# Performance work log

Hardware: AMD Instinct MI355X
Metric: run time of the kernel (lower is better)

## Reference

```python
import jax, jax.numpy as jnp
import numpy as np

# LSR-Patch tokenizer config (matches init_kwargs / torch defaults)
SPEC_WINDOW = 32
SPEC_HOP = 8
PELT_PENALTY = 1.0
PATCH_MIN = 8
PATCH_MAX = 64
PATCH_GRID = 2
ANCHOR_LEN = 16
ALPHA = 1.0
BETA = 1.0

B, C, L = 32, 64, 8192

# ---------------- host-side (numpy) planning: boundaries, segment stats, patch layout ----------------
# These produce integer index structures (non-differentiable in the torch original too:
# regime/center/span are built from python floats via torch.tensor -> constant leaves).

def _window_feats(agg):
    Ln = agg.shape[0]
    W = min(SPEC_WINDOW, Ln)
    if Ln <= W:
        starts = [0]
    else:
        starts = list(range(0, Ln - W + 1, SPEC_HOP))
        if starts[-1] != Ln - W:
            starts.append(Ln - W)
    s = np.asarray(starts)
    frames = agg[s[:, None] + np.arange(W)[None, :]]           # [n_win, W]
    p = np.abs(np.fft.rfft(frames, axis=1)) ** 2
    p = p[:, 1:]                                                # drop DC
    tot = np.maximum(p.sum(1), 1e-8)
    dom = np.argmax(p, 1) + 1
    f = np.arange(1, p.shape[1] + 1, dtype=np.float64)
    cent = (p * f).sum(1) / tot
    var = ((f[None, :] - cent[:, None]) ** 2 * p).sum(1) / tot
    bw = np.sqrt(np.maximum(var, 0.0)) / float(W)
    feat = np.stack([dom / float(W), bw, np.log1p(p.mean(1))], 1)
    return feat, starts

def _dp_changepoints(feat):
    # penalized DP (simplified PELT), O(n^2), vectorized inner minimization
    n, d = feat.shape
    pre = np.vstack([np.zeros((1, d)), np.cumsum(feat, 0)])
    pre2 = np.vstack([np.zeros((1, d)), np.cumsum(feat ** 2, 0)])
    dp = np.full(n + 1, np.inf)
    dp[0] = -PELT_PENALTY
    prev = np.full(n + 1, -1, np.int64)
    for end in range(1, n + 1):
        sl = (end - np.arange(end)).astype(np.float64)
        ssum = pre[end] - pre[:end]
        ssq = pre2[end] - pre2[:end]
        sse = (ssq - ssum ** 2 / sl[:, None]).sum(1)
        cand = dp[:end] + sse + PELT_PENALTY
        j = int(np.argmin(cand))
        dp[end] = cand[j]
        prev[end] = j
    bps = [n]
    i = n
    while i > 0:
        i = int(prev[i])
        bps.append(i)
    return bps[::-1]

def _detect_boundaries(agg):
    Ln = agg.shape[0]
    if Ln <= max(2, PATCH_MIN):
        return [0, Ln]
    feat, ws = _window_feats(agg)
    if feat.shape[0] <= 1:
        return [0, Ln]
    wb = _dp_changepoints(feat)
    bnd = [0]
    for w in wb[1:-1]:
        if w < 0 or w >= len(ws):
            continue
        t = int(ws[w])
        if t <= bnd[-1] or t - bnd[-1] < PATCH_MIN or Ln - t < PATCH_MIN:
            continue
        bnd.append(t)
    bnd.append(Ln)
    return bnd

def _segment_stats(seg):
    n = seg.shape[0]
    if n < 2:
        return 1.0, 0.0
    p = np.abs(np.fft.rfft(seg)) ** 2
    if p.size <= 1:
        return float(n), 0.0
    p = p[1:]
    tot = max(p.sum(), 1e-8)
    dom = int(np.argmax(p)) + 1
    f = np.arange(1, p.size + 1, dtype=np.float64)
    cent = (p * f).sum() / tot
    var = ((f - cent) ** 2 * p).sum() / tot
    bw = float(np.sqrt(max(var, 0.0)) / n)
    return float(n) / dom, bw

def _gen_patch_len(dom_period, bw, seg_len):
    # reconstruction of _generate_patch_length (truncated in source):
    # patch length ~ alpha*dom_period shrunk by bandwidth, snapped to grid, clamped
    raw = ALPHA * dom_period / (1.0 + BETA * bw)
    p = int(round(raw / PATCH_GRID)) * PATCH_GRID
    p = min(max(p, PATCH_MIN), PATCH_MAX)
    return max(1, p)

def _resize_plan(start, end):
    # F.interpolate(mode='linear', align_corners=False) gather indices + weights
    n = end - start
    A = ANCHOR_LEN
    src = (np.arange(A) + 0.5) * (n / float(A)) - 0.5
    src = np.clip(src, 0.0, n - 1.0)
    i0 = np.floor(src).astype(np.int64)
    i1 = np.minimum(i0 + 1, n - 1)
    w = (src - i0).astype(np.float32)
    return start + i0, start + i1, w

def _plan(x_np):
    Bn, Cn, Ln = x_np.shape
    plans = []
    mx = 0
    for b in range(Bn):
        agg = x_np[b].mean(0).astype(np.float64)
        bnd = _detect_boundaries(agg)
        i0s, i1s, ws, st, en, ce, sp, rg = [], [], [], [], [], [], [], []
        for s, e in zip(bnd[:-1], bnd[1:]):
            if e <= s:
                continue
            dom_p, bw = _segment_stats(agg[s:e])
            pl = _gen_patch_len(dom_p, bw, e - s)
            reg = [dom_p / float(max(Ln, 1)), bw, (e - s) / float(max(Ln, 1))]
            for a in range(s, e, pl):
                z = min(e, a + pl)
                if z <= a:
                    continue
                g0, g1, wv = _resize_plan(a, z)
                i0s.append(g0); i1s.append(g1); ws.append(wv)
                st.append(a); en.append(z)
                ce.append((a + z - 1) * 0.5 / float(Ln - 1) if Ln > 1 else 0.0)
                sp.append((z - a) / float(max(Ln, 1)))
                rg.append(reg)
        plans.append(dict(i0=np.stack(i0s), i1=np.stack(i1s), w=np.stack(ws),
                          start=np.asarray(st, np.int32), end=np.asarray(en, np.int32),
                          center=np.asarray(ce, np.float32), span=np.asarray(sp, np.float32),
                          regime=np.asarray(rg, np.float32), n=len(st)))
        mx = max(mx, len(st))
    return plans, mx

# ---------------- device-side (jnp) patch extraction: one batched gather+lerp per sample ----------------

def _patches(x, plans, mx):
    outs = []
    for b, p in enumerate(plans):
        w = jnp.asarray(p['w'])                                   # [n, A]
        g = x[b][:, p['i0']] * (1.0 - w) + x[b][:, p['i1']] * w    # [C, n, A]
        g = jnp.transpose(g, (1, 0, 2))                            # [n, C, A]
        outs.append(jnp.pad(g, ((0, mx - p['n']), (0, 0), (0, 0))))
    return jnp.stack(outs, 0)                                      # [B, mx, C, A]

def setup_inputs() -> dict:
    key = jax.random.key(0)
    x = jax.random.normal(key, (B, C, L), dtype=jnp.float32)
    return {"x": x}

def reference(x):
    xn = np.asarray(jax.device_get(x), dtype=np.float32)
    plans, mx = _plan(xn)
    patches = _patches(x, plans, mx)
    token_mask = jnp.stack([jnp.arange(mx) < p['n'] for p in plans], 0)
    start = jnp.stack([jnp.pad(jnp.asarray(p['start']), (0, mx - p['n'])) for p in plans], 0)
    end = jnp.stack([jnp.pad(jnp.asarray(p['end']), (0, mx - p['n'])) for p in plans], 0)
    center = jnp.stack([jnp.pad(jnp.asarray(p['center']), (0, mx - p['n'])) for p in plans], 0)[..., None]
    span = jnp.stack([jnp.pad(jnp.asarray(p['span']), (0, mx - p['n'])) for p in plans], 0)[..., None]
    regime = jnp.stack([jnp.pad(jnp.asarray(p['regime']), ((0, mx - p['n']), (0, 0))) for p in plans], 0)
    n_tokens = jnp.asarray([p['n'] for p in plans], dtype=jnp.int32)
    return (patches, token_mask, start, end, center, span, regime, n_tokens)
```

## Files before the change

### kernel.cpp

```cpp
#include <hip/hip_runtime.h>
#include <math.h>

#pragma clang fp contract(off)

#define BB 32
#define CC 64
#define LL 8192
#define NW 1021
#define MAXSEG 1024
#define MAXTOK 1024
#define BNDCAP 1026
#define NBINS (LL / 2)

#define DP_T 64
#define DP_NBLK 16
#define DP_NWAVE 16
#define DP_MARGIN 1e-6

template <typename F>
__device__ double np_pairwise(const F& f, int off, int n) {
  if (n < 8) {
    double res = 0.0;
    for (int i = 0; i < n; i++) res = res + f(off + i);
    return res;
  }
  if (n <= 128) {
    double r0 = f(off + 0), r1 = f(off + 1), r2 = f(off + 2), r3 = f(off + 3);
    double r4 = f(off + 4), r5 = f(off + 5), r6 = f(off + 6), r7 = f(off + 7);
    int i = 8;
    int lim = n - (n % 8);
    for (; i < lim; i += 8) {
      r0 = r0 + f(off + i + 0); r1 = r1 + f(off + i + 1);
      r2 = r2 + f(off + i + 2); r3 = r3 + f(off + i + 3);
      r4 = r4 + f(off + i + 4); r5 = r5 + f(off + i + 5);
      r6 = r6 + f(off + i + 6); r7 = r7 + f(off + i + 7);
    }
    double res = ((r0 + r1) + (r2 + r3)) + ((r4 + r5) + (r6 + r7));
    for (; i < n; i++) res = res + f(off + i);
    return res;
  }
  int n2 = n / 2;
  n2 -= n2 % 8;
  return np_pairwise(f, off, n2) + np_pairwise(f, off + n2, n - n2);
}

template <int KIND>
__device__ __noinline__ double wp_leaf(const double* __restrict__ pp, double cent,
                                       int off, int n, int lane) {
  int k = lane & 7;
  auto f = [&](int i) -> double {
    double pv = pp[i];
    if constexpr (KIND == 0) {
      return pv;
    } else if constexpr (KIND == 1) {
      return pv * (double)(i + 1);
    } else {
      double d = (double)(i + 1) - cent;
      double dd = d * d;
      return dd * pv;
    }
  };
  double r = f(off + k);
  int lim = n - (n % 8);
  for (int i = 8; i < lim; i += 8) r = r + f(off + i + k);
  double a = r + __shfl_xor(r, 1, 64);
  double b2 = a + __shfl_xor(a, 2, 64);
  double res = b2 + __shfl_xor(b2, 4, 64);
  for (int i = lim; i < n; i++) res = res + f(off + i);
  return res;
}

template <int DEPTH, int KIND>
__device__ double wp_tree(const double* __restrict__ pp, double cent, int off,
                          int n, int lane) {
  if (n <= 128) return wp_leaf<KIND>(pp, cent, off, n, lane);
  if constexpr (DEPTH > 0) {
    int n2 = n / 2;
    n2 -= n2 % 8;
    double l = wp_tree<DEPTH - 1, KIND>(pp, cent, off, n2, lane);
    double r = wp_tree<DEPTH - 1, KIND>(pp, cent, off + n2, n - n2, lane);
    return l + r;
  } else {
    if constexpr (KIND == 0)
      return np_pairwise([&](int i) { return pp[i]; }, off, n);
    else if constexpr (KIND == 1)
      return np_pairwise([&](int i) { return pp[i] * (double)(i + 1); }, off, n);
    else
      return np_pairwise(
          [&](int i) {
            double d = (double)(i + 1) - cent;
            double dd = d * d;
            return dd * pp[i];
          },
          off, n);
  }
}

__global__ void k_agg(const float* __restrict__ x, double* __restrict__ agg) {
  int idx = blockIdx.x * blockDim.x + threadIdx.x;
  if (idx >= BB * LL) return;
  int b = idx / LL, l = idx - b * LL;
  const float* xb = x + (size_t)b * CC * LL + l;
  float s = 0.0f;
  for (int c = 0; c < CC; c++) s = s + xb[(size_t)c * LL];
  agg[idx] = (double)(s / 64.0f);
}

__global__ void k_winfeat(const double* __restrict__ agg, double* __restrict__ feat) {
  __shared__ double tc[32], tsn[32];
  if (threadIdx.x < 32) {
    double th = 6.283185307179586 * ((double)threadIdx.x / 32.0);
    tc[threadIdx.x] = cos(th);
    tsn[threadIdx.x] = sin(th);
  }
  __syncthreads();
  int idx = blockIdx.x * blockDim.x + threadIdx.x;
  if (idx >= BB * NW) return;
  int b = idx / NW, w = idx - b * NW;
  const double* a = agg + (size_t)b * LL + (size_t)w * 8;
  double av[32];
#pragma unroll
  for (int t = 0; t < 32; t++) av[t] = a[t];
  double p[16];
  for (int k = 1; k <= 16; k++) {
    double re = 0.0, im = 0.0;
    int m = 0;
    for (int t = 0; t < 32; t++) {
      re = re + av[t] * tc[m];
      im = im + av[t] * tsn[m];
      m = (m + k) & 31;
    }
    p[k - 1] = re * re + im * im;
  }
  double r[8];
  for (int i = 0; i < 8; i++) r[i] = p[i] + p[i + 8];
  double sum = ((r[0] + r[1]) + (r[2] + r[3])) + ((r[4] + r[5]) + (r[6] + r[7]));
  double tot = (sum > 1e-8) ? sum : 1e-8;
  double pf[16];
  for (int i = 0; i < 16; i++) pf[i] = p[i] * (double)(i + 1);
  for (int i = 0; i < 8; i++) r[i] = pf[i] + pf[i + 8];
  double spf = ((r[0] + r[1]) + (r[2] + r[3])) + ((r[4] + r[5]) + (r[6] + r[7]));
  int dom = 0;
  double bv = p[0];
  for (int i = 1; i < 16; i++)
    if (p[i] > bv) { bv = p[i]; dom = i; }
  dom += 1;
  double cent = spf / tot;
  double q[16];
  for (int i = 0; i < 16; i++) {
    double d = (double)(i + 1) - cent;
    double dd = d * d;
    q[i] = dd * p[i];
  }
  for (int i = 0; i < 8; i++) r[i] = q[i] + q[i + 8];
  double sv = ((r[0] + r[1]) + (r[2] + r[3])) + ((r[4] + r[5]) + (r[6] + r[7]));
  double var = sv / tot;
  double bw = sqrt(var > 0.0 ? var : 0.0) / 32.0;
  double mean = sum / 16.0;
  double* f = feat + ((size_t)b * NW + (size_t)w) * 3;
  f[0] = (double)dom / 32.0;
  f[1] = bw;
  f[2] = log1p(mean);
}

__global__ __launch_bounds__(1024) void k_dp(const double* __restrict__ feat,
                                             int* __restrict__ bnd_g,
                                             int* __restrict__ nbnd_g,
                                             int* __restrict__ seg_s,
                                             int* __restrict__ seg_e,
                                             int* __restrict__ nseg_g) {
  __shared__ double cmb[NW + 1][8];
  __shared__ double sseT[2][DP_T][DP_T + 1];
  __shared__ double pvL[DP_T][DP_NWAVE + 1];
  __shared__ int pixL[DP_T][DP_NWAVE + 1];
  __shared__ int prevL[NW + 1];
  __shared__ double invL[NW + 1];
  int b = blockIdx.x;
  int tid = threadIdx.x;
  const double* fb = feat + (size_t)b * NW * 3;

  double* featS = &sseT[0][0][0];
  for (int i = tid; i < NW * 3; i += 1024) featS[i] = fb[i];
  for (int i = tid + 1; i <= NW; i += 1024) invL[i] = 1.0 / (double)i;
  if (tid == 0) {
    cmb[0][0] = 0.0; cmb[0][1] = 0.0; cmb[0][2] = 0.0;
    cmb[0][3] = 0.0;
    cmb[0][4] = -1.0;
    cmb[0][5] = 0.0; cmb[0][6] = 0.0; cmb[0][7] = 0.0;
  }
  __syncthreads();

  if (tid < 6) {
    int c = tid % 3;
    bool sq = tid >= 3;
    int col = sq ? 5 + c : c;
    double acc = 0.0;
    for (int i = 0; i < NW; i++) {
      double f = featS[i * 3 + c];
      double v = sq ? f * f : f;
      acc = acc + v;
      cmb[i + 1][col] = acc;
    }
  }
  __syncthreads();

  int lane = tid & 63;
  int w = tid >> 6;

  for (int i = tid + 1; i <= NW; i += 1024)
    cmb[i][3] = (cmb[i][5] + cmb[i][6]) + cmb[i][7];
  {
    int end = 1 + lane;
    double pe0 = cmb[end][0], pe1 = cmb[end][1], pe2 = cmb[end][2];
    double qe0 = cmb[end][5], qe1 = cmb[end][6], qe2 = cmb[end][7];
    for (int s = w; s < DP_T; s += DP_NWAVE) {
      int j = s;
      double sl = (double)(end - j);
      double s0 = pe0 - cmb[j][0], s1 = pe1 - cmb[j][1], s2 = pe2 - cmb[j][2];
      double u0 = s0 * s0, u1 = s1 * s1, u2 = s2 * s2;
      double t0 = (qe0 - cmb[j][5]) - u0 / sl;
      double t1 = (qe1 - cmb[j][6]) - u1 / sl;
      double t2 = (qe2 - cmb[j][7]) - u2 / sl;
      sseT[0][s][lane] = (t0 + t1) + t2;
    }
  }
  __syncthreads();

  double dpLast = -1.0;

  for (int blk = 0; blk < DP_NBLK; blk++) {
    int cur = blk & 1, nxt = cur ^ 1;
    int e0 = blk * DP_T;
    int ecnt = NW - e0;
    if (ecnt > DP_T) ecnt = DP_T;
    int end = e0 + 1 + lane;
    if (end > NW) end = NW;
    double pe0 = cmb[end][0], pe1 = cmb[end][1], pe2 = cmb[end][2];
    double qeS = cmb[end][3];
    double vminA = __builtin_inf();
    for (int j = w; j < e0; j += DP_NWAVE) {
      double p0 = cmb[j][0], p1 = cmb[j][1], p2 = cmb[j][2];
      double qs = cmb[j][3], dpj = cmb[j][4];
      double inv = invL[end - j];
      double s0 = pe0 - p0, s1 = pe1 - p1, s2 = pe2 - p2;
      double u0 = s0 * s0, u1 = s1 * s1, u2 = s2 * s2;
      double us = (u0 + u1) + u2;
      double ds = qeS - qs;
      double candA = (dpj + (ds - us * inv)) + 1.0;
      if (candA < vminA) vminA = candA;
    }
    pvL[lane][w] = vminA;
    __syncthreads();
    double mA = pvL[lane][0];
#pragma unroll
    for (int t = 1; t < DP_NWAVE; t++) {
      double ov = pvL[lane][t];
      if (ov < mA) mA = ov;
    }
    double thr = mA + DP_MARGIN;
    __syncthreads();
    double v = __builtin_inf();
    int ix = 0;
    for (int j = w; j < e0; j += DP_NWAVE) {
      double p0 = cmb[j][0], p1 = cmb[j][1], p2 = cmb[j][2];
      double qs = cmb[j][3], dpj = cmb[j][4];
      double inv = invL[end - j];
      double s0 = pe0 - p0, s1 = pe1 - p1, s2 = pe2 - p2;
      double u0 = s0 * s0, u1 = s1 * s1, u2 = s2 * s2;
      double us = (u0 + u1) + u2;
      double ds = qeS - qs;
      double candA = (dpj + (ds - us * inv)) + 1.0;
      if (candA <= thr) {
        double qe0 = cmb[end][5], qe1 = cmb[end][6], qe2 = cmb[end][7];
        double q0 = cmb[j][5], q1 = cmb[j][6], q2 = cmb[j][7];
        double sl = (double)(end - j);
        double t0 = (qe0 - q0) - u0 / sl;
        double t1 = (qe1 - q1) - u1 / sl;
        double t2 = (qe2 - q2) - u2 / sl;
        double cand = (dpj + ((t0 + t1) + t2)) + 1.0;
        if (cand < v || (cand == v && j < ix)) { v = cand; ix = j; }
      }
    }
    pvL[lane][w] = v;
    pixL[lane][w] = ix;
    __syncthreads();
    if (w == 0) {
      double vcur = pvL[lane][0];
      int ixcur = pixL[lane][0];
#pragma unroll
      for (int t = 1; t < DP_NWAVE; t++) {
        double ov = pvL[lane][t];
        int oi = pixL[lane][t];
        if (ov < vcur || (ov == vcur && oi < ixcur)) { vcur = ov; ixcur = oi; }
      }
      double sse_next = sseT[cur][0][lane];
      for (int s = 0; s < ecnt; s++) {
        double sse_cur = sse_next;
        if (s + 1 < ecnt) sse_next = sseT[cur][s + 1][lane];
        double dpj = (s == 0) ? dpLast : __shfl(vcur, s - 1, 64);
        double cand = (dpj + sse_cur) + 1.0;
        if (lane >= s && cand < vcur) { vcur = cand; ixcur = e0 + s; }
        if (lane == s) {
          cmb[end][4] = vcur;
          prevL[end] = ixcur;
        }
      }
      dpLast = __shfl(vcur, ecnt - 1, 64);
    } else if (blk + 1 < DP_NBLK) {
      int e0n = e0 + DP_T;
      int ecn = NW - e0n;
      if (ecn > DP_T) ecn = DP_T;
      int endn = e0n + 1 + lane;
      if (endn > NW) endn = NW;
      double pn0 = cmb[endn][0], pn1 = cmb[endn][1], pn2 = cmb[endn][2];
      double qn0 = cmb[endn][5], qn1 = cmb[endn][6], qn2 = cmb[endn][7];
      for (int s = w - 1; s < ecn; s += DP_NWAVE - 1) {
        int j = e0n + s;
        double sl = (double)(endn - j);
        double s0 = pn0 - cmb[j][0], s1 = pn1 - cmb[j][1], s2 = pn2 - cmb[j][2];
        double u0 = s0 * s0, u1 = s1 * s1, u2 = s2 * s2;
        double t0 = (qn0 - cmb[j][5]) - u0 / sl;
        double t1 = (qn1 - cmb[j][6]) - u1 / sl;
        double t2 = (qn2 - cmb[j][7]) - u2 / sl;
        sseT[nxt][s][lane] = (t0 + t1) + t2;
      }
    }
    __syncthreads();
  }

  if (tid == 0) {
    int* chain = (int*)cmb;
    int cnt = 0, i = NW;
    while (i > 0) { i = prevL[i]; chain[cnt++] = i; }
    int* bbL = (int*)invL;
    int nb = 0;
    bbL[nb++] = 0;
    for (int t = cnt - 2; t >= 0; t--) {
      int w2 = chain[t];
      int tt = w2 * 8;
      if (tt <= bbL[nb - 1]) continue;
      if (tt - bbL[nb - 1] < 8) continue;
      if (LL - tt < 8) continue;
      bbL[nb++] = tt;
    }
    bbL[nb++] = LL;
    int* bb = bnd_g + (size_t)b * BNDCAP;
    for (int t = 0; t < nb; t++) bb[t] = bbL[t];
    nbnd_g[b] = nb;
    int nseg = nb - 1;
    nseg_g[b] = nseg;
    for (int si = 0; si < nseg; si++) {
      seg_s[(size_t)b * MAXSEG + si] = bbL[si];
      seg_e[(size_t)b * MAXSEG + si] = bbL[si + 1];
    }
  }
}

__global__ __launch_bounds__(512) void k_bins(const double* __restrict__ agg,
                                              const int* __restrict__ bnd_g,
                                              const int* __restrict__ nbnd_g,
                                              double* __restrict__ segp) {
#pragma clang fp contract(fast)
  __shared__ int bbS[BNDCAP];
  __shared__ double reS[512], imS[512];
  int b = blockIdx.y;
  int nb = nbnd_g[b];
  for (int i = threadIdx.x; i < nb; i += 512) bbS[i] = bnd_g[(size_t)b * BNDCAP + i];
  __syncthreads();
  int gl = threadIdx.x & 255;
  int h = threadIdx.x >> 8;
  int g = blockIdx.x * 256 + gl;
  int pos = g * 2;
  int lo = 0, hi = nb - 1;
  while (hi - lo > 1) {
    int mid = (lo + hi) >> 1;
    if (bbS[mid] <= pos) lo = mid; else hi = mid;
  }
  int s = bbS[lo], e = bbS[lo + 1];
  int n = e - s;
  int k = g - s / 2 + 1;
  int m = n >> 1;
  const double* ab = agg + (size_t)b * LL + s + h * m;
  double th = 6.283185307179586 * ((double)k / (double)n);
  double cth = cos(th), sth = sin(th);
  double c2 = 2.0 * cth;
  double s1 = 0.0, s2 = 0.0;
  for (int t = m - 4; t >= 0; t -= 4) {
    double a0 = ab[t + 0], a1 = ab[t + 1], a2 = ab[t + 2], a3 = ab[t + 3];
    double x0 = (a3 - s2) + c2 * s1;
    double x1 = (a2 - s1) + c2 * x0;
    double x2 = (a1 - x0) + c2 * x1;
    double x3 = (a0 - x1) + c2 * x2;
    s2 = x2; s1 = x3;
  }
  double re = s1 - cth * s2;
  double im = sth * s2;
  reS[threadIdx.x] = re;
  imS[threadIdx.x] = im;
  __syncthreads();
  if (h == 0) {
    double re1 = reS[256 + gl], im1 = imS[256 + gl];
    double sgn = (k & 1) ? -1.0 : 1.0;
    double rr = re + sgn * re1;
    double ii = im + sgn * im1;
    segp[(size_t)b * NBINS + g] = rr * rr + ii * ii;
  }
}

__global__ __launch_bounds__(256) void k_segfin(
    const double* __restrict__ segp, const int* __restrict__ seg_s,
    const int* __restrict__ seg_e, const int* __restrict__ nseg_g,
    int* __restrict__ seg_pl, double* __restrict__ seg_domp,
    double* __restrict__ seg_bw) {
  __shared__ double ppS[NBINS];
  int b = blockIdx.x;
  for (int i = threadIdx.x; i < NBINS; i += 256) ppS[i] = segp[(size_t)b * NBINS + i];
  __syncthreads();
  int ns = nseg_g[b];
  int lane = threadIdx.x & 63;
  int wid = threadIdx.x >> 6;
  for (int si = wid; si < ns; si += 4) {
    int s = seg_s[(size_t)b * MAXSEG + si];
    int e = seg_e[(size_t)b * MAXSEG + si];
    int n = e - s;
    int nb2 = n / 2;
    int base = s / 2;
    double domp, bwv;
    if (n < 2) {
      domp = 1.0; bwv = 0.0;
    } else if (nb2 <= 1) {
      domp = (double)n; bwv = 0.0;
    } else {
      const double* pp = ppS + base;
      double sum, spf, sv;
      if (nb2 < 8) {
        sum = 0.0;
        for (int i = 0; i < nb2; i++) sum = sum + pp[i];
      } else {
        sum = wp_tree<7, 0>(pp, 0.0, 0, nb2, lane);
      }
      double tot = (sum > 1e-8) ? sum : 1e-8;
      int ch = (nb2 + 63) >> 6;
      double bv = -1.0;
      int bi = 0x7fffffff;
      int st = lane * ch;
      int en2 = st + ch;
      if (en2 > nb2) en2 = nb2;
      if (st < nb2) {
        bv = pp[st]; bi = st;
        for (int i = st + 1; i < en2; i++) {
          double pv = pp[i];
          if (pv > bv) { bv = pv; bi = i; }
        }
      }
      for (int o = 32; o; o >>= 1) {
        double ov = __shfl_xor(bv, o, 64);
        int oi = __shfl_xor(bi, o, 64);
        if (ov > bv || (ov == bv && oi < bi)) { bv = ov; bi = oi; }
      }
      int dom = bi + 1;
      if (nb2 < 8) {
        spf = 0.0;
        for (int i = 0; i < nb2; i++) spf = spf + pp[i] * (double)(i + 1);
      } else {
        spf = wp_tree<7, 1>(pp, 0.0, 0, nb2, lane);
      }
      double cent = spf / tot;
      if (nb2 < 8) {
        sv = 0.0;
        for (int i = 0; i < nb2; i++) {
          double d = (double)(i + 1) - cent;
          double dd = d * d;
          sv = sv + dd * pp[i];
        }
      } else {
        sv = wp_tree<7, 2>(pp, cent, 0, nb2, lane);
      }
      double var = sv / tot;
      bwv = sqrt(var > 0.0 ? var : 0.0) / (double)n;
      domp = (double)n / (double)dom;
    }
    double raw = (1.0 * domp) / (1.0 + 1.0 * bwv);
    int pl = (int)rint(raw / 2.0) * 2;
    if (pl < 8) pl = 8;
    if (pl > 64) pl = 64;
    if (lane == 0) {
      seg_pl[(size_t)b * MAXSEG + si] = pl;
      seg_domp[(size_t)b * MAXSEG + si] = domp;
      seg_bw[(size_t)b * MAXSEG + si] = bwv;
    }
  }
}

__global__ void k_tokens(const int* __restrict__ seg_s, const int* __restrict__ seg_e,
                         const int* __restrict__ seg_pl, const int* __restrict__ nseg_g,
                         int* __restrict__ tok_a, int* __restrict__ tok_z,
                         int* __restrict__ tok_sg, int* __restrict__ ntok_g,
                         float* __restrict__ out_nt) {
  int b = blockIdx.x * blockDim.x + threadIdx.x;
  if (b >= BB) return;
  int ns = nseg_g[b];
  int cnt = 0;
  for (int si = 0; si < ns; si++) {
    int s = seg_s[(size_t)b * MAXSEG + si];
    int e = seg_e[(size_t)b * MAXSEG + si];
    int pl = seg_pl[(size_t)b * MAXSEG + si];
    for (int a = s; a < e; a += pl) {
      int z = a + pl;
      if (z > e) z = e;
      tok_a[(size_t)b * MAXTOK + cnt] = a;
      tok_z[(size_t)b * MAXTOK + cnt] = z;
      tok_sg[(size_t)b * MAXTOK + cnt] = si;
      cnt++;
    }
  }
  ntok_g[b] = cnt;
  out_nt[b] = (float)cnt;
}

__global__ void k_tokfill(const int* __restrict__ tok_a, const int* __restrict__ tok_z,
                          const int* __restrict__ tok_sg, const int* __restrict__ ntok_g,
                          const int* __restrict__ seg_s, const int* __restrict__ seg_e,
                          const double* __restrict__ seg_domp,
                          const double* __restrict__ seg_bw, float* __restrict__ out,
                          int mx) {
  int b = blockIdx.x;
  int t = blockIdx.y * blockDim.x + threadIdx.x;
  if (t >= mx) return;
  size_t BM = (size_t)BB * (size_t)mx;
  float* mask = out + BM * 1024;
  float* start = mask + BM;
  float* endo = start + BM;
  float* cen = endo + BM;
  float* span = cen + BM;
  float* reg = span + BM;
  size_t o = (size_t)b * (size_t)mx + t;
  if (t >= ntok_g[b]) {
    mask[o] = 0.0f; start[o] = 0.0f; endo[o] = 0.0f;
    cen[o] = 0.0f; span[o] = 0.0f;
    reg[o * 3 + 0] = 0.0f; reg[o * 3 + 1] = 0.0f; reg[o * 3 + 2] = 0.0f;
    return;
  }
  int a = tok_a[(size_t)b * MAXTOK + t];
  int z = tok_z[(size_t)b * MAXTOK + t];
  int si = tok_sg[(size_t)b * MAXTOK + t];
  mask[o] = 1.0f;
  start[o] = (float)a;
  endo[o] = (float)z;
  cen[o] = (float)(((double)(a + z - 1) * 0.5) / 8191.0);
  span[o] = (float)((double)(z - a) / 8192.0);
  int s = seg_s[(size_t)b * MAXSEG + si];
  int e = seg_e[(size_t)b * MAXSEG + si];
  reg[o * 3 + 0] = (float)(seg_domp[(size_t)b * MAXSEG + si] / 8192.0);
  reg[o * 3 + 1] = (float)seg_bw[(size_t)b * MAXSEG + si];
  reg[o * 3 + 2] = (float)((double)(e - s) / 8192.0);
}

__global__ __launch_bounds__(256) void k_patches(const float* __restrict__ x,
                                                 const int* __restrict__ tok_a,
                                                 const int* __restrict__ tok_z,
                                                 const int* __restrict__ ntok_g,
                                                 float* __restrict__ out, int mx) {
  int t = blockIdx.x, b = blockIdx.y;
  float* ob = out + (((size_t)b * (size_t)mx + t) * CC) * 16;
  if (t >= ntok_g[b]) {
    for (int e2 = threadIdx.x; e2 < CC * 16; e2 += 256) ob[e2] = 0.0f;
    return;
  }
  __shared__ int g0[16], g1[16];
  __shared__ float wS[16];
  if (threadIdx.x < 16) {
    int a = tok_a[(size_t)b * MAXTOK + t];
    int z = tok_z[(size_t)b * MAXTOK + t];
    int n = z - a;
    double src = ((double)threadIdx.x + 0.5) * ((double)n / 16.0) - 0.5;
    if (src < 0.0) src = 0.0;
    double hi = (double)n - 1.0;
    if (src > hi) src = hi;
    double fi = floor(src);
    int i0 = (int)fi;
    int i1 = i0 + 1;
    if (i1 > n - 1) i1 = n - 1;
    g0[threadIdx.x] = a + i0;
    g1[threadIdx.x] = a + i1;
    wS[threadIdx.x] = (float)(src - fi);
  }
  __syncthreads();
  const float* xb = x + (size_t)b * CC * LL;
  for (int e2 = threadIdx.x; e2 < CC * 16; e2 += 256) {
    int c = e2 >> 4, ai = e2 & 15;
    float wv = wS[ai];
    float v0 = xb[(size_t)c * LL + g0[ai]];
    float v1 = xb[(size_t)c * LL + g1[ai]];
    ob[e2] = v0 * (1.0f - wv) + v1 * wv;
  }
}

extern "C" void kernel_launch(void* const* d_in, const int* in_sizes, int n_in,
                              void* d_out, int out_size, void* d_ws, size_t ws_size,
                              hipStream_t stream) {
  (void)in_sizes; (void)n_in; (void)ws_size;
  const float* x = (const float*)d_in[0];
  float* out = (float*)d_out;
  long mx = ((long)out_size / BB - 1) / 1032;
  if (mx < 1) mx = 1;

  char* wp = (char*)d_ws;
  size_t off = 0;
  auto carve = [&](size_t bytes) -> void* {
    void* p = wp + off;
    off += (bytes + 255) & ~(size_t)255;
    return p;
  };
  double* agg = (double*)carve((size_t)BB * LL * 8);
  double* feat = (double*)carve((size_t)BB * NW * 3 * 8);
  double* segp = (double*)carve((size_t)BB * NBINS * 8);
  double* seg_domp = (double*)carve((size_t)BB * MAXSEG * 8);
  double* seg_bw = (double*)carve((size_t)BB * MAXSEG * 8);
  int* bnd = (int*)carve((size_t)BB * BNDCAP * 4);
  int* nbnd = (int*)carve((size_t)BB * 4);
  int* seg_s = (int*)carve((size_t)BB * MAXSEG * 4);
  int* seg_e = (int*)carve((size_t)BB * MAXSEG * 4);
  int* seg_pl = (int*)carve((size_t)BB * MAXSEG * 4);
  int* nseg = (int*)carve((size_t)BB * 4);
  int* tok_a = (int*)carve((size_t)BB * MAXTOK * 4);
  int* tok_z = (int*)carve((size_t)BB * MAXTOK * 4);
  int* tok_sg = (int*)carve((size_t)BB * MAXTOK * 4);
  int* ntok = (int*)carve((size_t)BB * 4);

  k_agg<<<(BB * LL + 255) / 256, 256, 0, stream>>>(x, agg);
  k_winfeat<<<(BB * NW + 255) / 256, 256, 0, stream>>>(agg, feat);
  k_dp<<<BB, 1024, 0, stream>>>(feat, bnd, nbnd, seg_s, seg_e, nseg);
  dim3 gb(NBINS / 256, BB);
  k_bins<<<gb, 512, 0, stream>>>(agg, bnd, nbnd, segp);
  k_segfin<<<BB, 256, 0, stream>>>(segp, seg_s, seg_e, nseg, seg_pl, seg_domp,
                                   seg_bw);
  k_tokens<<<1, 64, 0, stream>>>(seg_s, seg_e, seg_pl, nseg, tok_a, tok_z,
                                 tok_sg, ntok, out + (size_t)BB * (size_t)mx * 1032);
  dim3 gf(BB, (unsigned)((mx + 255) / 256));
  k_tokfill<<<gf, 256, 0, stream>>>(tok_a, tok_z, tok_sg, ntok, seg_s, seg_e,
                                    seg_domp, seg_bw, out, (int)mx);
  dim3 gp((unsigned)mx, BB);
  k_patches<<<gp, 256, 0, stream>>>(x, tok_a, tok_z, ntok, out, (int)mx);
}
```

Measured before the change: 1.003 ms.

## Pipeline DP candidate scan for next block behind serial wave-0 recurrence

Restructures the blocked changepoint DP so the waves other than wave 0 compute the next block's candidate minima over already-finalized predecessors while wave 0 runs the serial in-block recurrence. The two barrier-separated scan passes per block go away. The current block's contributions are handled by 8 waves after the barrier. Precomputed per-j terms (dp+1-q sum) are folded into cmb[3], and a top-two screening step skips the exact re-evaluation when the best candidate is separated by more than the margin. This reduces barriers and redundant approximate-cost passes, but it adds FMA-based screening whose rounding could change tie-breaking relative to the reference.

```diff
diff --git a/kernel.cpp b/kernel.cpp
--- a/kernel.cpp
+++ b/kernel.cpp
@@ -14,7 +14,6 @@
 
 #define DP_T 64
 #define DP_NBLK 16
-#define DP_NWAVE 16
 #define DP_MARGIN 1e-6
 
 template <typename F>
@@ -170,9 +169,9 @@
                                              int* __restrict__ seg_e,
                                              int* __restrict__ nseg_g) {
   __shared__ double cmb[NW + 1][8];
-  __shared__ double sseT[2][DP_T][DP_T + 1];
-  __shared__ double pvL[DP_T][DP_NWAVE + 1];
-  __shared__ int pixL[DP_T][DP_NWAVE + 1];
+  __shared__ double sseT[2][DP_T][DP_T];
+  __shared__ double pvL[24][DP_T];
+  __shared__ int pixL[24][DP_T];
   __shared__ int prevL[NW + 1];
   __shared__ double invL[NW + 1];
   int b = blockIdx.x;
@@ -182,6 +181,10 @@
   double* featS = &sseT[0][0][0];
   for (int i = tid; i < NW * 3; i += 1024) featS[i] = fb[i];
   for (int i = tid + 1; i <= NW; i += 1024) invL[i] = 1.0 / (double)i;
+  for (int i = tid; i < 24 * DP_T; i += 1024) {
+    (&pvL[0][0])[i] = __builtin_inf();
+    (&pixL[0][0])[i] = 0;
+  }
   if (tid == 0) {
     cmb[0][0] = 0.0; cmb[0][1] = 0.0; cmb[0][2] = 0.0;
     cmb[0][3] = 0.0;
@@ -207,20 +210,17 @@
   int lane = tid & 63;
   int w = tid >> 6;
 
-  for (int i = tid + 1; i <= NW; i += 1024)
-    cmb[i][3] = (cmb[i][5] + cmb[i][6]) + cmb[i][7];
   {
     int end = 1 + lane;
     double pe0 = cmb[end][0], pe1 = cmb[end][1], pe2 = cmb[end][2];
     double qe0 = cmb[end][5], qe1 = cmb[end][6], qe2 = cmb[end][7];
-    for (int s = w; s < DP_T; s += DP_NWAVE) {
-      int j = s;
-      double sl = (double)(end - j);
-      double s0 = pe0 - cmb[j][0], s1 = pe1 - cmb[j][1], s2 = pe2 - cmb[j][2];
+    for (int s = w; s < DP_T; s += 16) {
+      double sl = (double)(end - s);
+      double s0 = pe0 - cmb[s][0], s1 = pe1 - cmb[s][1], s2 = pe2 - cmb[s][2];
       double u0 = s0 * s0, u1 = s1 * s1, u2 = s2 * s2;
-      double t0 = (qe0 - cmb[j][5]) - u0 / sl;
-      double t1 = (qe1 - cmb[j][6]) - u1 / sl;
-      double t2 = (qe2 - cmb[j][7]) - u2 / sl;
+      double t0 = (qe0 - cmb[s][5]) - u0 / sl;
+      double t1 = (qe1 - cmb[s][6]) - u1 / sl;
+      double t2 = (qe2 - cmb[s][7]) - u2 / sl;
       sseT[0][s][lane] = (t0 + t1) + t2;
     }
   }
@@ -233,66 +233,22 @@
     int e0 = blk * DP_T;
     int ecnt = NW - e0;
     if (ecnt > DP_T) ecnt = DP_T;
-    int end = e0 + 1 + lane;
-    if (end > NW) end = NW;
-    double pe0 = cmb[end][0], pe1 = cmb[end][1], pe2 = cmb[end][2];
-    double qeS = cmb[end][3];
-    double vminA = __builtin_inf();
-    for (int j = w; j < e0; j += DP_NWAVE) {
-      double p0 = cmb[j][0], p1 = cmb[j][1], p2 = cmb[j][2];
-      double qs = cmb[j][3], dpj = cmb[j][4];
-      double inv = invL[end - j];
-      double s0 = pe0 - p0, s1 = pe1 - p1, s2 = pe2 - p2;
-      double u0 = s0 * s0, u1 = s1 * s1, u2 = s2 * s2;
-      double us = (u0 + u1) + u2;
-      double ds = qeS - qs;
-      double candA = (dpj + (ds - us * inv)) + 1.0;
-      if (candA < vminA) vminA = candA;
-    }
-    pvL[lane][w] = vminA;
-    __syncthreads();
-    double mA = pvL[lane][0];
+    bool hasNext = (blk + 1 < DP_NBLK);
+    double vBig = __builtin_inf();
+    int ixBig = 0;
+
+    if (w == 0) {
+      int end = e0 + 1 + lane;
+      if (end > NW) end = NW;
+      double vcur = pvL[0][lane];
+      int ixcur = pixL[0][lane];
 #pragma unroll
-    for (int t = 1; t < DP_NWAVE; t++) {
-      double ov = pvL[lane][t];
-      if (ov < mA) mA = ov;
-    }
-    double thr = mA + DP_MARGIN;
-    __syncthreads();
-    double v = __builtin_inf();
-    int ix = 0;
-    for (int j = w; j < e0; j += DP_NWAVE) {
-      double p0 = cmb[j][0], p1 = cmb[j][1], p2 = cmb[j][2];
-      double qs = cmb[j][3], dpj = cmb[j][4];
-      double inv = invL[end - j];
-      double s0 = pe0 - p0, s1 = pe1 - p1, s2 = pe2 - p2;
-      double u0 = s0 * s0, u1 = s1 * s1, u2 = s2 * s2;
-      double us = (u0 + u1) + u2;
-      double ds = qeS - qs;
-      double candA = (dpj + (ds - us * inv)) + 1.0;
-      if (candA <= thr) {
-        double qe0 = cmb[end][5], qe1 = cmb[end][6], qe2 = cmb[end][7];
-        double q0 = cmb[j][5], q1 = cmb[j][6], q2 = cmb[j][7];
-        double sl = (double)(end - j);
-        double t0 = (qe0 - q0) - u0 / sl;
-        double t1 = (qe1 - q1) - u1 / sl;
-        double t2 = (qe2 - q2) - u2 / sl;
-        double cand = (dpj + ((t0 + t1) + t2)) + 1.0;
-        if (cand < v || (cand == v && j < ix)) { v = cand; ix = j; }
-      }
-    }
-    pvL[lane][w] = v;
-    pixL[lane][w] = ix;
-    __syncthreads();
-    if (w == 0) {
-      double vcur = pvL[lane][0];
-      int ixcur = pixL[lane][0];
-#pragma unroll
-      for (int t = 1; t < DP_NWAVE; t++) {
-        double ov = pvL[lane][t];
-        int oi = pixL[lane][t];
+      for (int t = 1; t < 23; t++) {
+        double ov = pvL[t][lane];
+        int oi = pixL[t][lane];
         if (ov < vcur || (ov == vcur && oi < ixcur)) { vcur = ov; ixcur = oi; }
       }
+      double qsE = (cmb[end][5] + cmb[end][6]) + cmb[end][7];
       double sse_next = sseT[cur][0][lane];
       for (int s = 0; s < ecnt; s++) {
         double sse_cur = sse_next;
@@ -303,10 +259,11 @@
         if (lane == s) {
           cmb[end][4] = vcur;
           prevL[end] = ixcur;
+          cmb[end][3] = (vcur + 1.0) - qsE;
         }
       }
       dpLast = __shfl(vcur, ecnt - 1, 64);
-    } else if (blk + 1 < DP_NBLK) {
+    } else if (hasNext) {
       int e0n = e0 + DP_T;
       int ecn = NW - e0n;
       if (ecn > DP_T) ecn = DP_T;
@@ -314,7 +271,7 @@
       if (endn > NW) endn = NW;
       double pn0 = cmb[endn][0], pn1 = cmb[endn][1], pn2 = cmb[endn][2];
       double qn0 = cmb[endn][5], qn1 = cmb[endn][6], qn2 = cmb[endn][7];
-      for (int s = w - 1; s < ecn; s += DP_NWAVE - 1) {
+      for (int s = w - 1; s < ecn; s += 15) {
         int j = e0n + s;
         double sl = (double)(endn - j);
         double s0 = pn0 - cmb[j][0], s1 = pn1 - cmb[j][1], s2 = pn2 - cmb[j][2];
@@ -323,6 +280,121 @@
         double t1 = (qn1 - cmb[j][6]) - u1 / sl;
         double t2 = (qn2 - cmb[j][7]) - u2 / sl;
         sseT[nxt][s][lane] = (t0 + t1) + t2;
+      }
+      double qeS = (qn0 + qn1) + qn2;
+      double m1 = __builtin_inf(), m2 = __builtin_inf();
+      int ix1 = -1;
+      for (int j = w - 1; j < e0; j += 15) {
+        double p0 = cmb[j][0], p1 = cmb[j][1], p2 = cmb[j][2], wj = cmb[j][3];
+        double inv = invL[endn - j];
+        double s0 = pn0 - p0, s1 = pn1 - p1, s2 = pn2 - p2;
+        double us = fma(s2, s2, fma(s1, s1, s0 * s0));
+        double candA = fma(-us, inv, wj + qeS);
+        if (candA < m1) { m2 = m1; m1 = candA; ix1 = j; }
+        else if (candA < m2) { m2 = candA; }
+      }
+      if (ix1 >= 0) {
+        if (m2 - m1 > DP_MARGIN) {
+          int j = ix1;
+          double p0 = cmb[j][0], p1 = cmb[j][1], p2 = cmb[j][2];
+          double q0 = cmb[j][5], q1 = cmb[j][6], q2 = cmb[j][7];
+          double dpj = cmb[j][4];
+          double sl = (double)(endn - j);
+          double s0 = pn0 - p0, s1 = pn1 - p1, s2 = pn2 - p2;
+          double u0 = s0 * s0, u1 = s1 * s1, u2 = s2 * s2;
+          double t0 = (qn0 - q0) - u0 / sl;
+          double t1 = (qn1 - q1) - u1 / sl;
+          double t2 = (qn2 - q2) - u2 / sl;
+          vBig = (dpj + ((t0 + t1) + t2)) + 1.0;
+          ixBig = j;
+        } else {
+          double thr = m1 + DP_MARGIN;
+          for (int j = w - 1; j < e0; j += 15) {
+            double p0 = cmb[j][0], p1 = cmb[j][1], p2 = cmb[j][2], wj = cmb[j][3];
+            double inv = invL[endn - j];
+            double s0 = pn0 - p0, s1 = pn1 - p1, s2 = pn2 - p2;
+            double us = fma(s2, s2, fma(s1, s1, s0 * s0));
+            double candA = fma(-us, inv, wj + qeS);
+            if (candA <= thr) {
+              double q0 = cmb[j][5], q1 = cmb[j][6], q2 = cmb[j][7];
+              double dpj = cmb[j][4];
+              double sl = (double)(endn - j);
+              double u0 = s0 * s0, u1 = s1 * s1, u2 = s2 * s2;
+              double t0 = (qn0 - q0) - u0 / sl;
+              double t1 = (qn1 - q1) - u1 / sl;
+              double t2 = (qn2 - q2) - u2 / sl;
+              double cand = (dpj + ((t0 + t1) + t2)) + 1.0;
+              if (cand < vBig || (cand == vBig && j < ixBig)) { vBig = cand; ixBig = j; }
+            }
+          }
+        }
+      }
+    }
+    __syncthreads();
+    if (hasNext) {
+      if (w >= 1) {
+        pvL[w - 1][lane] = vBig;
+        pixL[w - 1][lane] = ixBig;
+      }
+      if (w < 8) {
+        int e0n = e0 + DP_T;
+        int endn = e0n + 1 + lane;
+        if (endn > NW) endn = NW;
+        double pn0 = cmb[endn][0], pn1 = cmb[endn][1], pn2 = cmb[endn][2];
+        double qn0 = cmb[endn][5], qn1 = cmb[endn][6], qn2 = cmb[endn][7];
+        double qeS = (qn0 + qn1) + qn2;
+        double m1 = __builtin_inf(), m2 = __builtin_inf();
+        int ix1 = 0;
+        int j0 = e0 + w * 8;
+        for (int i = 0; i < 8; i++) {
+          int j = j0 + i;
+          double p0 = cmb[j][0], p1 = cmb[j][1], p2 = cmb[j][2], wj = cmb[j][3];
+          double inv = invL[endn - j];
+          double s0 = pn0 - p0, s1 = pn1 - p1, s2 = pn2 - p2;
+          double us = fma(s2, s2, fma(s1, s1, s0 * s0));
+          double candA = fma(-us, inv, wj + qeS);
+          if (candA < m1) { m2 = m1; m1 = candA; ix1 = j; }
+          else if (candA < m2) { m2 = candA; }
+        }
+        double v = __builtin_inf();
+        int ix = 0;
+        if (m2 - m1 > DP_MARGIN) {
+          int j = ix1;
+          double p0 = cmb[j][0], p1 = cmb[j][1], p2 = cmb[j][2];
+          double q0 = cmb[j][5], q1 = cmb[j][6], q2 = cmb[j][7];
+          double dpj = cmb[j][4];
+          double sl = (double)(endn - j);
+          double s0 = pn0 - p0, s1 = pn1 - p1, s2 = pn2 - p2;
+          double u0 = s0 * s0, u1 = s1 * s1, u2 = s2 * s2;
+          double t0 = (qn0 - q0) - u0 / sl;
+          double t1 = (qn1 - q1) - u1 / sl;
+          double t2 = (qn2 - q2) - u2 / sl;
+          v = (dpj + ((t0 + t1) + t2)) + 1.0;
+          ix = j;
+        } else {
+          double thr = m1 + DP_MARGIN;
+          for (int i = 0; i < 8; i++) {
+            int j = j0 + i;
+            double p0 = cmb[j][0], p1 = cmb[j][1], p2 = cmb[j][2], wj = cmb[j][3];
+            double inv = invL[endn - j];
+            double s0 = pn0 - p0, s1 = pn1 - p1, s2 = pn2 - p2;
+            double us = fma(s2, s2, fma(s1, s1, s0 * s0));
+            double candA = fma(-us, inv, wj + qeS);
+            if (candA <= thr) {
+              double q0 = cmb[j][5], q1 = cmb[j][6], q2 = cmb[j][7];
+              double dpj = cmb[j][4];
+              double sl = (double)(endn - j);
+              double u0 = s0 * s0, u1 = s1 * s1, u2 = s2 * s2;
+              double t0 = (qn0 - q0) - u0 / sl;
+              double t1 = (qn1 - q1) - u1 / sl;
+              double t2 = (qn2 - q2) - u2 / sl;
+              double cand = (dpj + ((t0 + t1) + t2)) + 1.0;
+              if (cand < v || (cand == v && j < ix)) { v = cand; ix = j; }
+            }
+          }
+        }
+        pvL[15 + w][lane] = v;
+        pixL[15 + w][lane] = ix;
       }
     }
     __syncthreads();
```

After: 868.0 us. 1.16x faster.
